# Performance work log

Measured on AMD Instinct MI355X. Metric: run time of the kernel, lower is better.

The kernel has to match this reference:

```python
import jax, jax.numpy as jnp
import numpy as np
jax.config.update('jax_enable_x64', True)  # hash arithmetic needs int64 like torch

MARGIN = 0.1
ALPHA = 1.0
BETA = 0.5
IDK_ID = 0
DEPTH = 3


def setup_inputs() -> dict:
    key = jax.random.key(0)
    k1, k2, k3, k4 = jax.random.split(key, 4)
    B, T, V = 2, 1024, 32000
    logits = jax.random.normal(k1, (B, T, V), dtype=jnp.float32)
    targets = jax.random.randint(k2, (B, T), 0, V, dtype=jnp.int64)
    inputs = jax.random.randint(k3, (B, T), 0, V, dtype=jnp.int64)
    salts = jax.random.randint(k4, (DEPTH, 1), 0, 1000000, dtype=jnp.int64)
    return {'logits': logits, 'targets': targets, 'inputs': inputs, 'salts': salts}


def reference(logits, targets, inputs, salts):
    B, T, V = logits.shape
    width = 2 * V
    flat_inputs = inputs.reshape(-1)    # (N,)
    flat_targets = targets.reshape(-1)  # (N,)

    # --- Count-min sketch: update (training=True) then query ---
    combined = flat_inputs * 31337 + flat_targets * 2654435769  # int64
    hashes = (combined[None, :] + salts) % width                 # (depth, N)
    # table starts at zeros; update = per-row bincount of hashes
    table = jax.vmap(lambda h: jnp.zeros((width,), jnp.float32).at[h].add(1.0))(hashes)
    basis_counts = jnp.min(jnp.take_along_axis(table, hashes, axis=1), axis=0)  # (N,)

    # --- lazy softmax ---
    p = jax.nn.softplus(logits)                          # (B,T,V)
    S = p.sum(axis=-1, keepdims=True)
    scale = jnp.minimum(1.0 / (S + 1e-6), 1.0)
    p_norm = p * scale
    remainder = jnp.maximum(1.0 - p_norm.sum(axis=-1, keepdims=True), 0.0)
    full_probs = p_norm.at[..., IDK_ID].add(remainder[..., 0])

    # --- NLL with ignore_index=-1 ---
    log_probs = jnp.log(jnp.maximum(full_probs, 1e-10))
    mask = (flat_targets != -1)
    tgt_safe = jnp.where(mask, flat_targets, 0)
    lp_t = jnp.take_along_axis(log_probs.reshape(-1, V), tgt_safe[:, None], axis=1)[:, 0]
    maskf = mask.astype(jnp.float32)
    nll_loss = -(lp_t * maskf).sum() / jnp.maximum(maskf.sum(), 1.0)

    # --- epistemic ranking loss ---
    basis_strength = jnp.tanh(basis_counts / 10.0)                       # (N,)
    p_target = jnp.take_along_axis(full_probs, targets[..., None], axis=-1)[..., 0]  # (B,T)
    p_idk = full_probs[..., IDK_ID]                                      # (B,T)
    ranking_error = jnp.maximum(p_idk - p_target + MARGIN, 0.0)
    basis_loss = (ranking_error * basis_strength.reshape(B, T)).mean()

    return ALPHA * nll_loss + BETA * basis_loss
```

## Files before the change

kernel.cpp:

```cpp
#include <hip/hip_runtime.h>

constexpr int Vn     = 32000;
constexpr int Nn     = 2048;
constexpr int DEPTHn = 3;
constexpr int WIDTHn = 2 * Vn;

__device__ inline float softplus_f(float x) {
    return fmaxf(x, 0.0f) + __logf(1.0f + __expf(-fabsf(x)));
}

__global__ void sketch_update_kernel(const int* __restrict__ targets,
                                     const int* __restrict__ inputs,
                                     const int* __restrict__ salts,
                                     int* __restrict__ table) {
    int i = blockIdx.x * blockDim.x + threadIdx.x;
    if (i >= Nn) return;
    long long combined = (long long)inputs[i] * 31337LL +
                         (long long)targets[i] * 2654435769LL;
#pragma unroll
    for (int d = 0; d < DEPTHn; ++d) {
        int h = (int)((combined + (long long)salts[d]) % (long long)WIDTHn);
        atomicAdd(&table[d * WIDTHn + h], 1);
    }
}

__global__ __launch_bounds__(256)
void row_kernel(const float* __restrict__ logits,
                const int* __restrict__ targets,
                const int* __restrict__ inputs,
                const int* __restrict__ salts,
                const int* __restrict__ table,
                float* __restrict__ nll_arr,
                float* __restrict__ rank_arr) {
    const int row = blockIdx.x;
    const float* lr = logits + (size_t)row * Vn;
    const float4* l4 = reinterpret_cast<const float4*>(lr);

    float local = 0.0f;
    for (int j = threadIdx.x; j < Vn / 4; j += 256) {
        float4 v = l4[j];
        local += softplus_f(v.x) + softplus_f(v.y) + softplus_f(v.z) + softplus_f(v.w);
    }

#pragma unroll
    for (int off = 32; off > 0; off >>= 1)
        local += __shfl_down(local, off, 64);
    __shared__ float smem[4];
    if ((threadIdx.x & 63) == 0) smem[threadIdx.x >> 6] = local;
    __syncthreads();

    if (threadIdx.x == 0) {
        float S = smem[0] + smem[1] + smem[2] + smem[3];
        float scale = fminf(1.0f / (S + 1e-6f), 1.0f);
        float remainder = fmaxf(1.0f - S * scale, 0.0f);

        int tgt = targets[row];
        bool mask = (tgt != -1);
        int tsafe = mask ? tgt : 0;

        float pt = softplus_f(lr[tsafe]) * scale + (tsafe == 0 ? remainder : 0.0f);
        float p0 = softplus_f(lr[0]) * scale + remainder;

        float lp_t = __logf(fmaxf(pt, 1e-10f));
        nll_arr[row] = mask ? -lp_t : 0.0f;

        long long combined = (long long)inputs[row] * 31337LL +
                             (long long)tgt * 2654435769LL;
        int c = 0x7fffffff;
#pragma unroll
        for (int d = 0; d < DEPTHn; ++d) {
            int h = (int)((combined + (long long)salts[d]) % (long long)WIDTHn);
            c = min(c, table[d * WIDTHn + h]);
        }
        float strength = tanhf((float)c * 0.1f);
        float rerr = fmaxf(p0 - pt + 0.1f, 0.0f);
        rank_arr[row] = rerr * strength;
    }
}

__global__ __launch_bounds__(256)
void finalize_kernel(const float* __restrict__ nll_arr,
                     const float* __restrict__ rank_arr,
                     const int* __restrict__ targets,
                     float* __restrict__ out) {
    float nll = 0.0f, rank = 0.0f, cnt = 0.0f;
    for (int i = threadIdx.x; i < Nn; i += 256) {
        nll += nll_arr[i];
        rank += rank_arr[i];
        cnt += (targets[i] != -1) ? 1.0f : 0.0f;
    }
#pragma unroll
    for (int off = 32; off > 0; off >>= 1) {
        nll  += __shfl_down(nll, off, 64);
        rank += __shfl_down(rank, off, 64);
        cnt  += __shfl_down(cnt, off, 64);
    }
    __shared__ float sn[4], sr[4], sc[4];
    if ((threadIdx.x & 63) == 0) {
        int w = threadIdx.x >> 6;
        sn[w] = nll; sr[w] = rank; sc[w] = cnt;
    }
    __syncthreads();
    if (threadIdx.x == 0) {
        float tn = sn[0] + sn[1] + sn[2] + sn[3];
        float tr = sr[0] + sr[1] + sr[2] + sr[3];
        float tc = sc[0] + sc[1] + sc[2] + sc[3];
        float nll_loss   = tn / fmaxf(tc, 1.0f);
        float basis_loss = tr / (float)Nn;
        out[0] = 1.0f * nll_loss + 0.5f * basis_loss;
    }
}

extern "C" void kernel_launch(void* const* d_in, const int* in_sizes, int n_in,
                              void* d_out, int out_size, void* d_ws, size_t ws_size,
                              hipStream_t stream) {
    const float* logits  = (const float*)d_in[0];
    const int*   targets = (const int*)d_in[1];
    const int*   inputs  = (const int*)d_in[2];
    const int*   salts   = (const int*)d_in[3];

    int*   table    = (int*)d_ws;
    float* nll_arr  = (float*)((char*)d_ws + (size_t)DEPTHn * WIDTHn * sizeof(int));
    float* rank_arr = nll_arr + Nn;

    hipMemsetAsync(d_ws, 0, (size_t)DEPTHn * WIDTHn * sizeof(int), stream);
    sketch_update_kernel<<<(Nn + 255) / 256, 256, 0, stream>>>(targets, inputs, salts, table);
    row_kernel<<<Nn, 256, 0, stream>>>(logits, targets, inputs, salts, table,
                                       nll_arr, rank_arr);
    finalize_kernel<<<1, 256, 0, stream>>>(nll_arr, rank_arr, targets, (float*)d_out);
}
```

Before: 371.5 us.

## Replace count-min sketch with per-row exact hash-collision counting in shared memory

Drops the table memset, the sketch-update kernel and the salts. Each row block now hashes all tokens into shared memory and counts collisions with its own hash. This works because a salt shifts every hash equally, so collisions are the same at every depth and the minimum is just the collision count. The 64-bit hash is reduced to 32-bit unsigned maths with the multiplier pre-reduced mod the width; this is only correct while the values stay nonnegative and small enough not to wrap. In exchange, every block repeats O(N) hashing work.

```diff
diff --git a/kernel.cpp b/kernel.cpp
--- a/kernel.cpp
+++ b/kernel.cpp
@@ -1,40 +1,30 @@
 #include <hip/hip_runtime.h>
 
-constexpr int Vn     = 32000;
-constexpr int Nn     = 2048;
-constexpr int DEPTHn = 3;
-constexpr int WIDTHn = 2 * Vn;
+constexpr int Vn = 32000;
+constexpr int Nn = 2048;
+constexpr unsigned WIDTHu = 64000u;
+
 
 __device__ inline float softplus_f(float x) {
     return fmaxf(x, 0.0f) + __logf(1.0f + __expf(-fabsf(x)));
-}
-
-__global__ void sketch_update_kernel(const int* __restrict__ targets,
-                                     const int* __restrict__ inputs,
-                                     const int* __restrict__ salts,
-                                     int* __restrict__ table) {
-    int i = blockIdx.x * blockDim.x + threadIdx.x;
-    if (i >= Nn) return;
-    long long combined = (long long)inputs[i] * 31337LL +
-                         (long long)targets[i] * 2654435769LL;
-#pragma unroll
-    for (int d = 0; d < DEPTHn; ++d) {
-        int h = (int)((combined + (long long)salts[d]) % (long long)WIDTHn);
-        atomicAdd(&table[d * WIDTHn + h], 1);
-    }
 }
 
 __global__ __launch_bounds__(256)
 void row_kernel(const float* __restrict__ logits,
                 const int* __restrict__ targets,
                 const int* __restrict__ inputs,
-                const int* __restrict__ salts,
-                const int* __restrict__ table,
                 float* __restrict__ nll_arr,
                 float* __restrict__ rank_arr) {
     const int row = blockIdx.x;
     const float* lr = logits + (size_t)row * Vn;
     const float4* l4 = reinterpret_cast<const float4*>(lr);
+
+    __shared__ unsigned short cm_s[Nn];
+
+    for (int j = threadIdx.x; j < Nn; j += 256) {
+        unsigned s = (unsigned)inputs[j] * 31337u + (unsigned)targets[j] * 35769u;
+        cm_s[j] = (unsigned short)(s % WIDTHu);
+    }
 
     float local = 0.0f;
     for (int j = threadIdx.x; j < Vn / 4; j += 256) {
@@ -42,15 +32,31 @@
         local += softplus_f(v.x) + softplus_f(v.y) + softplus_f(v.z) + softplus_f(v.w);
     }
 
+    __syncthreads();
+
+    unsigned my = (unsigned)inputs[row] * 31337u + (unsigned)targets[row] * 35769u;
+    const unsigned short myc = (unsigned short)(my % WIDTHu);
+    int cnt = 0;
+    for (int j = threadIdx.x; j < Nn; j += 256)
+        cnt += (cm_s[j] == myc) ? 1 : 0;
+
 #pragma unroll
-    for (int off = 32; off > 0; off >>= 1)
+    for (int off = 32; off > 0; off >>= 1) {
         local += __shfl_down(local, off, 64);
+        cnt   += __shfl_down(cnt, off, 64);
+    }
     __shared__ float smem[4];
-    if ((threadIdx.x & 63) == 0) smem[threadIdx.x >> 6] = local;
+    __shared__ int   scnt[4];
+    if ((threadIdx.x & 63) == 0) {
+        smem[threadIdx.x >> 6] = local;
+        scnt[threadIdx.x >> 6] = cnt;
+    }
     __syncthreads();
 
     if (threadIdx.x == 0) {
         float S = smem[0] + smem[1] + smem[2] + smem[3];
+        int   c = scnt[0] + scnt[1] + scnt[2] + scnt[3];
+
         float scale = fminf(1.0f / (S + 1e-6f), 1.0f);
         float remainder = fmaxf(1.0f - S * scale, 0.0f);
 
@@ -64,14 +70,6 @@
         float lp_t = __logf(fmaxf(pt, 1e-10f));
         nll_arr[row] = mask ? -lp_t : 0.0f;
 
-        long long combined = (long long)inputs[row] * 31337LL +
-                             (long long)tgt * 2654435769LL;
-        int c = 0x7fffffff;
-#pragma unroll
-        for (int d = 0; d < DEPTHn; ++d) {
-            int h = (int)((combined + (long long)salts[d]) % (long long)WIDTHn);
-            c = min(c, table[d * WIDTHn + h]);
-        }
         float strength = tanhf((float)c * 0.1f);
         float rerr = fmaxf(p0 - pt + 0.1f, 0.0f);
         rank_arr[row] = rerr * strength;
@@ -117,15 +115,10 @@
     const float* logits  = (const float*)d_in[0];
     const int*   targets = (const int*)d_in[1];
     const int*   inputs  = (const int*)d_in[2];
-    const int*   salts   = (const int*)d_in[3];
 
-    int*   table    = (int*)d_ws;
-    float* nll_arr  = (float*)((char*)d_ws + (size_t)DEPTHn * WIDTHn * sizeof(int));
+    float* nll_arr  = (float*)d_ws;
     float* rank_arr = nll_arr + Nn;
 
-    hipMemsetAsync(d_ws, 0, (size_t)DEPTHn * WIDTHn * sizeof(int), stream);
-    sketch_update_kernel<<<(Nn + 255) / 256, 256, 0, stream>>>(targets, inputs, salts, table);
-    row_kernel<<<Nn, 256, 0, stream>>>(logits, targets, inputs, salts, table,
-                                       nll_arr, rank_arr);
+    row_kernel<<<Nn, 256, 0, stream>>>(logits, targets, inputs, nll_arr, rank_arr);
     finalize_kernel<<<1, 256, 0, stream>>>(nll_arr, rank_arr, targets, (float*)d_out);
 }
```

New measurement: 366.4 us. No clear change (-1.4%).
